# Optimization experiments

Measured on AMD Instinct MI355X. Metric: run time of the kernel, lower is better.

## Reference

```python
import jax, jax.numpy as jnp
import numpy as np

N = 50000      # nodes
E = 800000     # edges per relation
R = 2          # relations
L = 2          # conv layers
D = 128        # hidden / input channels
G = 64         # graphs in batch
C = 8          # num_classes


def setup_inputs() -> dict:
    key = jax.random.key(0)
    ks = jax.random.split(key, 6)
    x = jax.random.normal(ks[0], (N, D), dtype=jnp.float32)
    W = jax.random.normal(ks[1], (L, R, D, D), dtype=jnp.float32) * 0.05
    b = jnp.zeros((L, R, D), dtype=jnp.float32)
    lin_w = jax.random.normal(ks[2], (D, C), dtype=jnp.float32) * 0.05
    lin_b = jnp.zeros((C,), dtype=jnp.float32)
    edge_index = jax.random.randint(ks[3], (R, 2, E), 0, N, dtype=jnp.int32)
    batch = jnp.sort(jax.random.randint(ks[4], (N,), 0, G, dtype=jnp.int32))
    return {"x": x, "W": W, "b": b, "lin_w": lin_w, "lin_b": lin_b,
            "edge_index": edge_index, "batch": batch}


def _gcn_conv(x, src, dst, inv_sqrt_deg, W_r, b_r):
    """PyG GCNConv: symmetric-normalized aggregation with self loops.
    out[i] = sum_{j->i} d_i^-1/2 d_j^-1/2 (x_j W) + d_i^-1 (x_i W) + b
    where d includes the self loop (in-degree + 1)."""
    xw = x @ W_r                                   # [N, D]
    norm = inv_sqrt_deg[src] * inv_sqrt_deg[dst]   # [E]
    agg = jax.ops.segment_sum(xw[src] * norm[:, None], dst, num_segments=N)
    agg = agg + xw * (inv_sqrt_deg * inv_sqrt_deg)[:, None]  # self-loop msg
    return agg + b_r


def reference(x, W, b, lin_w, lin_b, edge_index, batch):
    # Pre-compute per-relation symmetric normalization (same for all layers).
    inv_sqrt_degs = []
    for r in range(R):
        dst = edge_index[r, 1]
        deg = jax.ops.segment_sum(jnp.ones((E,), x.dtype), dst, num_segments=N) + 1.0
        inv_sqrt_degs.append(jax.lax.rsqrt(deg))

    h = x
    for l in range(L):
        out = jnp.zeros((N, D), x.dtype)
        for r in range(R):  # HeteroConv aggr='sum' over relations
            out = out + _gcn_conv(h, edge_index[r, 0], edge_index[r, 1],
                                  inv_sqrt_degs[r], W[l, r], b[l, r])
        h = jax.nn.relu(out) if l < L - 1 else out

    # global_mean_pool over batch ids
    counts = jax.ops.segment_sum(jnp.ones((N,), x.dtype), batch, num_segments=G)
    sums = jax.ops.segment_sum(h, batch, num_segments=G)
    pooled = sums / jnp.maximum(counts, 1.0)[:, None]   # [G, D]
    # dropout(p=0.5) is identity in eval mode; final Linear
    return pooled @ lin_w + lin_b                        # [G, C]
```

## Files before the change

kernel.cpp:

```cpp
#include <hip/hip_runtime.h>
#include <math.h>

#define NN 50000
#define EE 800000
#define RR 2
#define LL 2
#define DD 128
#define GG 64
#define CCLS 8
#define NBUK 196
#define BCAP 6144

typedef unsigned int uint;
typedef unsigned short ushort;
typedef short bf16x8 __attribute__((ext_vector_type(8)));
typedef float f32x4 __attribute__((ext_vector_type(4)));
typedef float f32x2 __attribute__((ext_vector_type(2)));

#define OFF_XW    ((size_t)0)
#define OFF_H1    ((size_t)12800000)
#define OFF_WBT   ((size_t)25600000)
#define OFF_ISD   ((size_t)25731072)
#define OFF_RP    ((size_t)26131072)
#define OFF_CI    ((size_t)26531136)
#define OFF_BD    ((size_t)32931136)
#define OFF_ZERO  ((size_t)42564928)
#define ZO_GCUR 0
#define ZO_SUM  1600
#define ZO_CNT  34368
#define ZERO_BYTES 34624

static __device__ __forceinline__ ushort f2b(float f) {
  uint u = __float_as_uint(f);
  uint r = (u + 0x7fffu + ((u >> 16) & 1u)) >> 16;
  return (ushort)r;
}
static __device__ __forceinline__ float blo(uint u) { return __uint_as_float(u << 16); }
static __device__ __forceinline__ float bhi(uint u) { return __uint_as_float(u & 0xffff0000u); }

__global__ __launch_bounds__(256) void k_wprep(const float* __restrict__ W,
                                               ushort* __restrict__ WT) {
  int idx = blockIdx.x * 256 + threadIdx.x;
  int lr = idx >> 14;
  int rem = idx & 16383;
  int n = rem >> 7, k = rem & 127;
  WT[lr * 16384 + n * 128 + k] = f2b(W[lr * 16384 + k * 128 + n]);
}

__global__ __launch_bounds__(256) void k_part(const int* __restrict__ EI,
                                              int* __restrict__ gcur,
                                              uint* __restrict__ bdata) {
  __shared__ int hist[256];
  __shared__ int sbase[256];
  __shared__ int gbase[256];
  __shared__ int lcur[256];
  __shared__ uint stage[4096];
  __shared__ unsigned char bstage[4096];
  const int r = blockIdx.y;
  const int t = threadIdx.x;
  const int e0 = blockIdx.x * 4096;
  const int cnt = min(4096, EE - e0);
  hist[t] = 0;
  lcur[t] = 0;
  __syncthreads();

  int src[16], dst[16];
  bool val[4];
#pragma unroll
  for (int j = 0; j < 4; ++j) {
    int i4 = (j * 256 + t) * 4;
    val[j] = (i4 < cnt);
    if (val[j]) {
      int4 s4 = *(const int4*)(EI + (size_t)r * 2 * EE + e0 + i4);
      int4 d4 = *(const int4*)(EI + (size_t)r * 2 * EE + EE + e0 + i4);
      src[j * 4 + 0] = s4.x; src[j * 4 + 1] = s4.y; src[j * 4 + 2] = s4.z; src[j * 4 + 3] = s4.w;
      dst[j * 4 + 0] = d4.x; dst[j * 4 + 1] = d4.y; dst[j * 4 + 2] = d4.z; dst[j * 4 + 3] = d4.w;
#pragma unroll
      for (int i = 0; i < 4; ++i) atomicAdd(&hist[dst[j * 4 + i] >> 8], 1);
    }
  }
  __syncthreads();
  int hv = hist[t];
  if (t < NBUK && hv > 0)
    gbase[t] = atomicAdd(&gcur[r * NBUK + t], hv);
  else
    gbase[t] = 0;
  sbase[t] = hv;
  __syncthreads();
  for (int off = 1; off < 256; off <<= 1) {
    int u = (t >= off) ? sbase[t - off] : 0;
    __syncthreads();
    sbase[t] += u;
    __syncthreads();
  }
  int incl = sbase[t];
  hist[t] = incl - hv;
  __syncthreads();
#pragma unroll
  for (int j = 0; j < 4; ++j) {
    if (val[j]) {
#pragma unroll
      for (int i = 0; i < 4; ++i) {
        int d = dst[j * 4 + i];
        int b = d >> 8;
        int p = atomicAdd(&lcur[b], 1);
        int pos = hist[b] + p;
        stage[pos] = ((uint)src[j * 4 + i] << 8) | (uint)(d & 255);
        bstage[pos] = (unsigned char)b;
      }
    }
  }
  __syncthreads();
  for (int s = t; s < cnt; s += 256) {
    int b = (int)bstage[s];
    bdata[(size_t)(r * NBUK + b) * BCAP + gbase[b] + (s - hist[b])] = stage[s];
  }
}

__global__ __launch_bounds__(256) void k_csr(const uint* __restrict__ bdata,
                                             const int* __restrict__ gcur,
                                             float* __restrict__ isd,
                                             int* __restrict__ rp,
                                             int* __restrict__ ci) {
  __shared__ int lcnt[256];
  __shared__ int lrp[256];
  __shared__ int lcur[256];
  __shared__ int cstage[BCAP];
  __shared__ int basesh;
  const int b = blockIdx.x;
  const int r = blockIdx.y;
  const int t = threadIdx.x;
  const int cnt = gcur[r * NBUK + b];
  lcnt[t] = (t < b) ? gcur[r * NBUK + t] : 0;
  __syncthreads();
  for (int off = 128; off > 0; off >>= 1) {
    if (t < off) lcnt[t] += lcnt[t + off];
    __syncthreads();
  }
  if (t == 0) basesh = lcnt[0];
  __syncthreads();
  const int base = basesh;
  const uint* bd = bdata + (size_t)(r * NBUK + b) * BCAP;
  __syncthreads();
  lcnt[t] = 0;
  lcur[t] = 0;
  __syncthreads();
  for (int s = t; s < cnt; s += 256) {
    uint pr = bd[s];
    atomicAdd(&lcnt[pr & 255u], 1);
  }
  __syncthreads();
  int deg = lcnt[t];
  lrp[t] = deg;
  __syncthreads();
  for (int off = 1; off < 256; off <<= 1) {
    int u = (t >= off) ? lrp[t - off] : 0;
    __syncthreads();
    lrp[t] += u;
    __syncthreads();
  }
  int incl = lrp[t];
  __syncthreads();
  lrp[t] = incl - deg;
  __syncthreads();
  int node = b * 256 + t;
  if (node < NN) {
    isd[r * NN + node] = rsqrtf((float)(deg + 1));
    rp[r * (NN + 1) + node] = base + lrp[t];
  }
  if (b == NBUK - 1 && t == 0) rp[r * (NN + 1) + NN] = EE;
  for (int s = t; s < cnt; s += 256) {
    uint pr = bd[s];
    int j = (int)(pr & 255u);
    int p = atomicAdd(&lcur[j], 1);
    cstage[lrp[j] + p] = (int)(pr >> 8);
  }
  __syncthreads();
  for (int s = t; s < cnt; s += 256) ci[(size_t)r * EE + base + s] = cstage[s];
}

#define AL_S 72
#define WT_S 136
template <int IN_BF16>
__global__ __launch_bounds__(256) void k_gemm(const void* __restrict__ Xv,
                                              const ushort* __restrict__ WTg,
                                              const float* __restrict__ isd,
                                              uint* __restrict__ Y) {
  __shared__ ushort WTl[128 * WT_S];
  __shared__ ushort Al[128 * AL_S];
  const int r = blockIdx.y;
  const int m0b = blockIdx.x * 128;
  const int t = threadIdx.x;
  const int w = t >> 6, L = t & 63, q = L >> 4, ln = L & 15;
  uint* Yr = Y + (size_t)r * NN * 32;
  const ushort* WTr = WTg + (size_t)r * 16384;

#pragma unroll
  for (int i = 0; i < 8; ++i) {
    int g = t + i * 256;
    int n = g >> 4, k0 = (g & 15) * 8;
    *(uint4*)(&WTl[n * WT_S + k0]) = *(const uint4*)(WTr + n * 128 + k0);
  }

  f32x4 acc[2][8];
#pragma unroll
  for (int mt = 0; mt < 2; ++mt)
#pragma unroll
    for (int nt = 0; nt < 8; ++nt) {
      acc[mt][nt][0] = 0.f; acc[mt][nt][1] = 0.f;
      acc[mt][nt][2] = 0.f; acc[mt][nt][3] = 0.f;
    }

  for (int hh = 0; hh < 2; ++hh) {
    __syncthreads();
    {
      int row = t >> 1, ch = t & 1;
      int gm = m0b + row;
      ushort* dst = &Al[row * AL_S + ch * 32];
      if (gm < NN) {
        if (IN_BF16) {
          const uint4* xp = (const uint4*)((const ushort*)Xv + (size_t)gm * 128 + hh * 64 + ch * 32);
#pragma unroll
          for (int j = 0; j < 4; ++j) ((uint4*)dst)[j] = xp[j];
        } else {
          const float4* xp = (const float4*)((const float*)Xv + (size_t)gm * 128 + hh * 64 + ch * 32);
          ushort tmp[32];
#pragma unroll
          for (int j = 0; j < 8; ++j) {
            float4 v = xp[j];
            tmp[j * 4 + 0] = f2b(v.x); tmp[j * 4 + 1] = f2b(v.y);
            tmp[j * 4 + 2] = f2b(v.z); tmp[j * 4 + 3] = f2b(v.w);
          }
#pragma unroll
          for (int j = 0; j < 4; ++j) ((uint4*)dst)[j] = ((uint4*)tmp)[j];
        }
      } else {
        uint4 z = make_uint4(0, 0, 0, 0);
#pragma unroll
        for (int j = 0; j < 4; ++j) ((uint4*)dst)[j] = z;
      }
    }
    __syncthreads();
#pragma unroll
    for (int kk = 0; kk < 2; ++kk) {
      bf16x8 b0 = *(const bf16x8*)(&Al[(w * 32 + ln) * AL_S + kk * 32 + q * 8]);
      bf16x8 b1 = *(const bf16x8*)(&Al[(w * 32 + 16 + ln) * AL_S + kk * 32 + q * 8]);
#pragma unroll
      for (int nt = 0; nt < 8; ++nt) {
        bf16x8 a = *(const bf16x8*)(&WTl[(nt * 16 + ln) * WT_S + hh * 64 + kk * 32 + q * 8]);
        acc[0][nt] = __builtin_amdgcn_mfma_f32_16x16x32_bf16(a, b0, acc[0][nt], 0, 0, 0);
        acc[1][nt] = __builtin_amdgcn_mfma_f32_16x16x32_bf16(a, b1, acc[1][nt], 0, 0, 0);
      }
    }
  }
#pragma unroll
  for (int mt = 0; mt < 2; ++mt) {
    int m = m0b + w * 32 + mt * 16 + ln;
    if (m < NN) {
      float sc = isd[r * NN + m];
      uint* yp = Yr + (size_t)m * 32;
#pragma unroll
      for (int nt = 0; nt < 8; ++nt) {
        f32x4 v = acc[mt][nt];
        uint u = __builtin_amdgcn_cvt_pk_fp8_f32(v[0] * sc, v[1] * sc, 0u, false);
        u = __builtin_amdgcn_cvt_pk_fp8_f32(v[2] * sc, v[3] * sc, u, true);
        yp[nt * 4 + q] = u;
      }
    }
  }
}

__global__ __launch_bounds__(256) void k_agg(const uint4* __restrict__ xw4,
                                             const int* __restrict__ rp,
                                             const int* __restrict__ ci,
                                             const float* __restrict__ isd,
                                             const float* __restrict__ bias,
                                             uint* __restrict__ hout, int relu_flag) {
  const int w = threadIdx.x >> 6;
  const int lane = threadIdx.x & 63;
  const int g = lane >> 3, c = lane & 7;
  const int i = blockIdx.x * 4 + w;

  float tot[16];
#pragma unroll
  for (int k = 0; k < 16; ++k) tot[k] = 0.f;

#pragma unroll
  for (int r = 0; r < RR; ++r) {
    const uint4* xwr = xw4 + (size_t)r * NN * 8;
    const int* cir = ci + (size_t)r * EE;
    const float di = isd[r * NN + i];
    const int e0 = rp[r * (NN + 1) + i];
    const int cnt = rp[r * (NN + 1) + i + 1] - e0;
    const int total = cnt + 1;

    float acc[16];
#pragma unroll
    for (int k = 0; k < 16; ++k) acc[k] = 0.f;

    int s_cur = (g < cnt) ? cir[e0 + g] : i;
    for (int base = 0; base < total; base += 8) {
      int idxn = base + 8 + g;
      int s_next = (idxn < cnt) ? cir[e0 + idxn] : i;
      if (base + g < total) {
        uint4 u = xwr[(size_t)s_cur * 8 + c];
        f32x2 v;
        v = __builtin_amdgcn_cvt_pk_f32_fp8(u.x, false); acc[0] += v[0];  acc[1] += v[1];
        v = __builtin_amdgcn_cvt_pk_f32_fp8(u.x, true);  acc[2] += v[0];  acc[3] += v[1];
        v = __builtin_amdgcn_cvt_pk_f32_fp8(u.y, false); acc[4] += v[0];  acc[5] += v[1];
        v = __builtin_amdgcn_cvt_pk_f32_fp8(u.y, true);  acc[6] += v[0];  acc[7] += v[1];
        v = __builtin_amdgcn_cvt_pk_f32_fp8(u.z, false); acc[8] += v[0];  acc[9] += v[1];
        v = __builtin_amdgcn_cvt_pk_f32_fp8(u.z, true);  acc[10] += v[0]; acc[11] += v[1];
        v = __builtin_amdgcn_cvt_pk_f32_fp8(u.w, false); acc[12] += v[0]; acc[13] += v[1];
        v = __builtin_amdgcn_cvt_pk_f32_fp8(u.w, true);  acc[14] += v[0]; acc[15] += v[1];
      }
      s_cur = s_next;
    }
#pragma unroll
    for (int k = 0; k < 16; ++k) tot[k] = fmaf(di, acc[k], tot[k]);
  }

#pragma unroll
  for (int mask = 8; mask <= 32; mask <<= 1) {
#pragma unroll
    for (int k = 0; k < 16; ++k) tot[k] += __shfl_xor(tot[k], mask);
  }

  if (g < 2) {
    int ch0 = c * 16 + g * 8;
    const float4* bp = (const float4*)(bias + ch0);
    const float4* bq = (const float4*)(bias + DD + ch0);
    float4 b0 = bp[0], b1 = bp[1], b2 = bq[0], b3 = bq[1];
    float o[8];
#pragma unroll
    for (int j = 0; j < 8; ++j) o[j] = (g == 0) ? tot[j] : tot[8 + j];
    o[0] += b0.x + b2.x; o[1] += b0.y + b2.y; o[2] += b0.z + b2.z; o[3] += b0.w + b2.w;
    o[4] += b1.x + b3.x; o[5] += b1.y + b3.y; o[6] += b1.z + b3.z; o[7] += b1.w + b3.w;
    if (relu_flag) {
#pragma unroll
      for (int j = 0; j < 8; ++j) o[j] = fmaxf(o[j], 0.f);
    }
    uint4 pk;
    pk.x = (uint)f2b(o[0]) | ((uint)f2b(o[1]) << 16);
    pk.y = (uint)f2b(o[2]) | ((uint)f2b(o[3]) << 16);
    pk.z = (uint)f2b(o[4]) | ((uint)f2b(o[5]) << 16);
    pk.w = (uint)f2b(o[6]) | ((uint)f2b(o[7]) << 16);
    ((uint4*)(hout + (size_t)i * 64))[c * 2 + g] = pk;
  }
}

#define PCHUNK 32
__global__ __launch_bounds__(64) void k_pool(const uint* __restrict__ h,
                                             const int* __restrict__ batch,
                                             float* __restrict__ sums,
                                             int* __restrict__ counts) {
  int lane = threadIdx.x;
  int n0 = blockIdx.x * PCHUNK;
  int n1 = n0 + PCHUNK;
  if (n1 > NN) n1 = NN;
  if (n0 >= NN) return;
  float aLo = 0.f, aHi = 0.f;
  int cnt = 0;
  int g = batch[n0];
  uint u = h[(size_t)n0 * 64 + lane];
  for (int n = n0; n < n1; ++n) {
    uint unext = 0;
    int gnext = g;
    if (n + 1 < n1) {
      unext = h[(size_t)(n + 1) * 64 + lane];
      gnext = batch[n + 1];
    }
    aLo += blo(u);
    aHi += bhi(u);
    cnt++;
    if (n + 1 < n1 && gnext != g) {
      atomicAdd(&sums[g * DD + lane * 2], aLo);
      atomicAdd(&sums[g * DD + lane * 2 + 1], aHi);
      if (lane == 0) atomicAdd(&counts[g], cnt);
      aLo = 0.f; aHi = 0.f; cnt = 0;
      g = gnext;
    }
    u = unext;
  }
  atomicAdd(&sums[g * DD + lane * 2], aLo);
  atomicAdd(&sums[g * DD + lane * 2 + 1], aHi);
  if (lane == 0) atomicAdd(&counts[g], cnt);
}

__global__ __launch_bounds__(512) void k_final(const float* __restrict__ sums,
                                               const int* __restrict__ counts,
                                               const float* __restrict__ lin_w,
                                               const float* __restrict__ lin_b,
                                               float* __restrict__ out) {
  int t = threadIdx.x;
  int g = t >> 3, co = t & 7;
  float cnt = (float)counts[g];
  if (cnt < 1.f) cnt = 1.f;
  float inv = 1.f / cnt;
  float v = lin_b[co];
  for (int d = 0; d < DD; ++d) v += (sums[g * DD + d] * inv) * lin_w[d * CCLS + co];
  out[t] = v;
}

extern "C" void kernel_launch(void* const* d_in, const int* in_sizes, int n_in,
                              void* d_out, int out_size, void* d_ws, size_t ws_size,
                              hipStream_t stream) {
  (void)in_sizes; (void)n_in; (void)out_size; (void)ws_size;
  const float* x     = (const float*)d_in[0];
  const float* W     = (const float*)d_in[1];
  const float* b     = (const float*)d_in[2];
  const float* lin_w = (const float*)d_in[3];
  const float* lin_b = (const float*)d_in[4];
  const int*   EI    = (const int*)d_in[5];
  const int*   batch = (const int*)d_in[6];
  float* out = (float*)d_out;

  char* ws = (char*)d_ws;
  uint*   xw    = (uint*)(ws + OFF_XW);
  uint*   h1    = (uint*)(ws + OFF_H1);
  ushort* WbfT  = (ushort*)(ws + OFF_WBT);
  float*  isd   = (float*)(ws + OFF_ISD);
  int*    rp    = (int*)(ws + OFF_RP);
  int*    ci    = (int*)(ws + OFF_CI);
  uint*   bdata = (uint*)(ws + OFF_BD);
  char*   zb    = ws + OFF_ZERO;
  int*    gcur  = (int*)(zb + ZO_GCUR);
  float*  sums  = (float*)(zb + ZO_SUM);
  int*    counts= (int*)(zb + ZO_CNT);

  (void)hipMemsetAsync(zb, 0, ZERO_BYTES, stream);

  k_wprep<<<256, 256, 0, stream>>>(W, WbfT);
  k_part<<<dim3((EE + 4095) / 4096, RR), 256, 0, stream>>>(EI, gcur, bdata);
  k_csr<<<dim3(NBUK, RR), 256, 0, stream>>>(bdata, gcur, isd, rp, ci);

  for (int l = 0; l < LL; ++l) {
    const ushort* WTl_g = WbfT + (size_t)l * RR * DD * DD;
    if (l == 0)
      k_gemm<0><<<dim3((NN + 127) / 128, RR), 256, 0, stream>>>((const void*)x, WTl_g, isd, xw);
    else
      k_gemm<1><<<dim3((NN + 127) / 128, RR), 256, 0, stream>>>((const void*)h1, WTl_g, isd, xw);
    k_agg<<<(NN + 3) / 4, 256, 0, stream>>>((const uint4*)xw, rp, ci, isd,
                                            b + (size_t)l * RR * DD, h1,
                                            (l < LL - 1) ? 1 : 0);
  }
  k_pool<<<(NN + PCHUNK - 1) / PCHUNK, 64, 0, stream>>>(h1, batch, sums, counts);
  k_final<<<1, GG * CCLS, 0, stream>>>(sums, counts, lin_w, lin_b, out);
}
```

Measured before the change: 258.5 us.

## Pad CSR rows to multiples of four with a zero dummy node and branchless gather

The CSR build now pads each node's neighbour list, including the self loop, to a multiple of four, using a dummy node NN whose transformed row is written as zero by the GEMM. Each bucket gets a fixed-stride region, so the global prefix over buckets is removed. The aggregation kernel uses 16 lanes per edge with 8-byte fp8 loads over 4 edges per step, without bounds checks, and pipelines the next index and row load. The cost is extra padded gathers and larger index storage; the xw buffer also now shares its workspace with the bucket staging area.

Result: slower. 289.3 us (+11.9%).

```diff
diff --git a/kernel.cpp b/kernel.cpp
--- a/kernel.cpp
+++ b/kernel.cpp
@@ -10,6 +10,7 @@
 #define CCLS 8
 #define NBUK 196
 #define BCAP 6144
+#define BCI  7424
 
 typedef unsigned int uint;
 typedef unsigned short ushort;
@@ -17,14 +18,14 @@
 typedef float f32x4 __attribute__((ext_vector_type(4)));
 typedef float f32x2 __attribute__((ext_vector_type(2)));
 
-#define OFF_XW    ((size_t)0)
-#define OFF_H1    ((size_t)12800000)
-#define OFF_WBT   ((size_t)25600000)
-#define OFF_ISD   ((size_t)25731072)
-#define OFF_RP    ((size_t)26131072)
-#define OFF_CI    ((size_t)26531136)
-#define OFF_BD    ((size_t)32931136)
-#define OFF_ZERO  ((size_t)42564928)
+#define OFF_H1    ((size_t)0)
+#define OFF_WBT   ((size_t)12800000)
+#define OFF_ISD   ((size_t)12931072)
+#define OFF_RP    ((size_t)13331072)
+#define OFF_CI    ((size_t)14131072)
+#define OFF_ZERO  ((size_t)25771904)
+#define OFF_BD    ((size_t)25806592)
+#define OFF_XW    ((size_t)25806592)
 #define ZO_GCUR 0
 #define ZO_SUM  1600
 #define ZO_CNT  34368
@@ -120,38 +121,29 @@
 __global__ __launch_bounds__(256) void k_csr(const uint* __restrict__ bdata,
                                              const int* __restrict__ gcur,
                                              float* __restrict__ isd,
-                                             int* __restrict__ rp,
+                                             int* __restrict__ rps,
+                                             int* __restrict__ rpc,
                                              int* __restrict__ ci) {
   __shared__ int lcnt[256];
   __shared__ int lrp[256];
   __shared__ int lcur[256];
-  __shared__ int cstage[BCAP];
-  __shared__ int basesh;
+  __shared__ int cstage[BCI];
+  __shared__ int shtot;
   const int b = blockIdx.x;
   const int r = blockIdx.y;
   const int t = threadIdx.x;
   const int cnt = gcur[r * NBUK + b];
-  lcnt[t] = (t < b) ? gcur[r * NBUK + t] : 0;
-  __syncthreads();
-  for (int off = 128; off > 0; off >>= 1) {
-    if (t < off) lcnt[t] += lcnt[t + off];
-    __syncthreads();
-  }
-  if (t == 0) basesh = lcnt[0];
-  __syncthreads();
-  const int base = basesh;
   const uint* bd = bdata + (size_t)(r * NBUK + b) * BCAP;
-  __syncthreads();
   lcnt[t] = 0;
   lcur[t] = 0;
   __syncthreads();
-  for (int s = t; s < cnt; s += 256) {
-    uint pr = bd[s];
-    atomicAdd(&lcnt[pr & 255u], 1);
-  }
-  __syncthreads();
-  int deg = lcnt[t];
-  lrp[t] = deg;
+  for (int s = t; s < cnt; s += 256) atomicAdd(&lcnt[bd[s] & 255u], 1);
+  __syncthreads();
+  const int deg = lcnt[t];
+  const int node = b * 256 + t;
+  const int valid = (node < NN) ? 1 : 0;
+  const int deg3 = valid ? ((deg + 1 + 3) & ~3) : 0;
+  lrp[t] = deg3;
   __syncthreads();
   for (int off = 1; off < 256; off <<= 1) {
     int u = (t >= off) ? lrp[t - off] : 0;
@@ -160,15 +152,21 @@
     __syncthreads();
   }
   int incl = lrp[t];
-  __syncthreads();
-  lrp[t] = incl - deg;
-  __syncthreads();
-  int node = b * 256 + t;
-  if (node < NN) {
+  if (t == 255) shtot = incl;
+  __syncthreads();
+  lrp[t] = incl - deg3;
+  __syncthreads();
+  const int ex = lrp[t];
+  if (valid) {
     isd[r * NN + node] = rsqrtf((float)(deg + 1));
-    rp[r * (NN + 1) + node] = base + lrp[t];
-  }
-  if (b == NBUK - 1 && t == 0) rp[r * (NN + 1) + NN] = EE;
+    rps[r * NN + node] = b * BCI + ex;
+    rpc[r * NN + node] = deg3;
+    cstage[ex + deg] = node;
+    for (int p = deg + 1; p < deg3; ++p) cstage[ex + p] = NN;
+  }
+  const int btot = shtot;
+  if (t < 16) cstage[btot + t] = NN;
+  __syncthreads();
   for (int s = t; s < cnt; s += 256) {
     uint pr = bd[s];
     int j = (int)(pr & 255u);
@@ -176,7 +174,9 @@
     cstage[lrp[j] + p] = (int)(pr >> 8);
   }
   __syncthreads();
-  for (int s = t; s < cnt; s += 256) ci[(size_t)r * EE + base + s] = cstage[s];
+  const int on = btot + 16;
+  int* co = ci + (size_t)r * (NBUK * BCI) + (size_t)b * BCI;
+  for (int s = t; s < on; s += 256) co[s] = cstage[s];
 }
 
 #define AL_S 72
@@ -192,7 +192,7 @@
   const int m0b = blockIdx.x * 128;
   const int t = threadIdx.x;
   const int w = t >> 6, L = t & 63, q = L >> 4, ln = L & 15;
-  uint* Yr = Y + (size_t)r * NN * 32;
+  uint* Yr = Y + (size_t)r * (NN + 1) * 32;
   const ushort* WTr = WTg + (size_t)r * 16384;
 
 #pragma unroll
@@ -256,8 +256,8 @@
 #pragma unroll
   for (int mt = 0; mt < 2; ++mt) {
     int m = m0b + w * 32 + mt * 16 + ln;
-    if (m < NN) {
-      float sc = isd[r * NN + m];
+    if (m <= NN) {
+      float sc = (m < NN) ? isd[r * NN + m] : 0.f;
       uint* yp = Yr + (size_t)m * 32;
 #pragma unroll
       for (int nt = 0; nt < 8; ++nt) {
@@ -270,72 +270,76 @@
   }
 }
 
-__global__ __launch_bounds__(256) void k_agg(const uint4* __restrict__ xw4,
-                                             const int* __restrict__ rp,
+__global__ __launch_bounds__(256) void k_agg(const char* __restrict__ xw,
+                                             const int* __restrict__ rps,
+                                             const int* __restrict__ rpc,
                                              const int* __restrict__ ci,
                                              const float* __restrict__ isd,
                                              const float* __restrict__ bias,
                                              uint* __restrict__ hout, int relu_flag) {
   const int w = threadIdx.x >> 6;
   const int lane = threadIdx.x & 63;
-  const int g = lane >> 3, c = lane & 7;
+  const int g = lane >> 4, c = lane & 15;
   const int i = blockIdx.x * 4 + w;
-
-  float tot[16];
-#pragma unroll
-  for (int k = 0; k < 16; ++k) tot[k] = 0.f;
+  const uint cb = (uint)c * 8u;
+
+  f32x2 tot[4];
+#pragma unroll
+  for (int j = 0; j < 4; ++j) { tot[j][0] = 0.f; tot[j][1] = 0.f; }
 
 #pragma unroll
   for (int r = 0; r < RR; ++r) {
-    const uint4* xwr = xw4 + (size_t)r * NN * 8;
-    const int* cir = ci + (size_t)r * EE;
+    const char* xwr = xw + (size_t)r * ((size_t)(NN + 1) * 128);
+    const int e0 = rps[r * NN + i];
+    const int total = rpc[r * NN + i];
+    const int* ce = ci + (size_t)r * (NBUK * BCI) + e0;
     const float di = isd[r * NN + i];
-    const int e0 = rp[r * (NN + 1) + i];
-    const int cnt = rp[r * (NN + 1) + i + 1] - e0;
-    const int total = cnt + 1;
-
-    float acc[16];
-#pragma unroll
-    for (int k = 0; k < 16; ++k) acc[k] = 0.f;
-
-    int s_cur = (g < cnt) ? cir[e0 + g] : i;
-    for (int base = 0; base < total; base += 8) {
-      int idxn = base + 8 + g;
-      int s_next = (idxn < cnt) ? cir[e0 + idxn] : i;
-      if (base + g < total) {
-        uint4 u = xwr[(size_t)s_cur * 8 + c];
-        f32x2 v;
-        v = __builtin_amdgcn_cvt_pk_f32_fp8(u.x, false); acc[0] += v[0];  acc[1] += v[1];
-        v = __builtin_amdgcn_cvt_pk_f32_fp8(u.x, true);  acc[2] += v[0];  acc[3] += v[1];
-        v = __builtin_amdgcn_cvt_pk_f32_fp8(u.y, false); acc[4] += v[0];  acc[5] += v[1];
-        v = __builtin_amdgcn_cvt_pk_f32_fp8(u.y, true);  acc[6] += v[0];  acc[7] += v[1];
-        v = __builtin_amdgcn_cvt_pk_f32_fp8(u.z, false); acc[8] += v[0];  acc[9] += v[1];
-        v = __builtin_amdgcn_cvt_pk_f32_fp8(u.z, true);  acc[10] += v[0]; acc[11] += v[1];
-        v = __builtin_amdgcn_cvt_pk_f32_fp8(u.w, false); acc[12] += v[0]; acc[13] += v[1];
-        v = __builtin_amdgcn_cvt_pk_f32_fp8(u.w, true);  acc[14] += v[0]; acc[15] += v[1];
-      }
-      s_cur = s_next;
-    }
-#pragma unroll
-    for (int k = 0; k < 16; ++k) tot[k] = fmaf(di, acc[k], tot[k]);
-  }
-
-#pragma unroll
-  for (int mask = 8; mask <= 32; mask <<= 1) {
-#pragma unroll
-    for (int k = 0; k < 16; ++k) tot[k] += __shfl_xor(tot[k], mask);
-  }
-
-  if (g < 2) {
-    int ch0 = c * 16 + g * 8;
-    const float4* bp = (const float4*)(bias + ch0);
-    const float4* bq = (const float4*)(bias + DD + ch0);
-    float4 b0 = bp[0], b1 = bp[1], b2 = bq[0], b3 = bq[1];
-    float o[8];
-#pragma unroll
-    for (int j = 0; j < 8; ++j) o[j] = (g == 0) ? tot[j] : tot[8 + j];
-    o[0] += b0.x + b2.x; o[1] += b0.y + b2.y; o[2] += b0.z + b2.z; o[3] += b0.w + b2.w;
-    o[4] += b1.x + b3.x; o[5] += b1.y + b3.y; o[6] += b1.z + b3.z; o[7] += b1.w + b3.w;
+
+    f32x2 acc[4];
+#pragma unroll
+    for (int j = 0; j < 4; ++j) { acc[j][0] = 0.f; acc[j][1] = 0.f; }
+
+    int s0 = ce[g];
+    uint2 ucur = *(const uint2*)(xwr + (((uint)s0 << 7) + cb));
+    int s1 = ce[4 + g];
+    int ip = 8 + g;
+    for (int base = 0; base < total; base += 4) {
+      uint2 unext = *(const uint2*)(xwr + (((uint)s1 << 7) + cb));
+      int s2 = ce[ip];
+      ip += 4;
+      f32x2 v;
+      v = __builtin_amdgcn_cvt_pk_f32_fp8(ucur.x, false); acc[0] += v;
+      v = __builtin_amdgcn_cvt_pk_f32_fp8(ucur.x, true);  acc[1] += v;
+      v = __builtin_amdgcn_cvt_pk_f32_fp8(ucur.y, false); acc[2] += v;
+      v = __builtin_amdgcn_cvt_pk_f32_fp8(ucur.y, true);  acc[3] += v;
+      ucur = unext;
+      s1 = s2;
+    }
+    f32x2 d2; d2[0] = di; d2[1] = di;
+#pragma unroll
+    for (int j = 0; j < 4; ++j) tot[j] += acc[j] * d2;
+  }
+
+#pragma unroll
+  for (int mask = 16; mask <= 32; mask <<= 1) {
+#pragma unroll
+    for (int j = 0; j < 4; ++j) {
+      f32x2 o;
+      o[0] = __shfl_xor(tot[j][0], mask);
+      o[1] = __shfl_xor(tot[j][1], mask);
+      tot[j] += o;
+    }
+  }
+
+  if (g == 0) {
+    const int ch0 = c * 8;
+    const float4* b0p = (const float4*)(bias + ch0);
+    const float4* b1p = (const float4*)(bias + DD + ch0);
+    float4 ba = b0p[0], bb = b0p[1], bc = b1p[0], bd = b1p[1];
+    float o[8] = {tot[0][0], tot[0][1], tot[1][0], tot[1][1],
+                  tot[2][0], tot[2][1], tot[3][0], tot[3][1]};
+    o[0] += ba.x + bc.x; o[1] += ba.y + bc.y; o[2] += ba.z + bc.z; o[3] += ba.w + bc.w;
+    o[4] += bb.x + bd.x; o[5] += bb.y + bd.y; o[6] += bb.z + bd.z; o[7] += bb.w + bd.w;
     if (relu_flag) {
 #pragma unroll
       for (int j = 0; j < 8; ++j) o[j] = fmaxf(o[j], 0.f);
@@ -345,7 +349,7 @@
     pk.y = (uint)f2b(o[2]) | ((uint)f2b(o[3]) << 16);
     pk.z = (uint)f2b(o[4]) | ((uint)f2b(o[5]) << 16);
     pk.w = (uint)f2b(o[6]) | ((uint)f2b(o[7]) << 16);
-    ((uint4*)(hout + (size_t)i * 64))[c * 2 + g] = pk;
+    ((uint4*)(hout + (size_t)i * 64))[c] = pk;
   }
 }
 
@@ -416,13 +420,14 @@
   float* out = (float*)d_out;
 
   char* ws = (char*)d_ws;
-  uint*   xw    = (uint*)(ws + OFF_XW);
   uint*   h1    = (uint*)(ws + OFF_H1);
   ushort* WbfT  = (ushort*)(ws + OFF_WBT);
   float*  isd   = (float*)(ws + OFF_ISD);
-  int*    rp    = (int*)(ws + OFF_RP);
+  int*    rps   = (int*)(ws + OFF_RP);
+  int*    rpc   = rps + 2 * NN;
   int*    ci    = (int*)(ws + OFF_CI);
   uint*   bdata = (uint*)(ws + OFF_BD);
+  uint*   xw    = (uint*)(ws + OFF_XW);
   char*   zb    = ws + OFF_ZERO;
   int*    gcur  = (int*)(zb + ZO_GCUR);
   float*  sums  = (float*)(zb + ZO_SUM);
@@ -432,7 +437,7 @@
 
   k_wprep<<<256, 256, 0, stream>>>(W, WbfT);
   k_part<<<dim3((EE + 4095) / 4096, RR), 256, 0, stream>>>(EI, gcur, bdata);
-  k_csr<<<dim3(NBUK, RR), 256, 0, stream>>>(bdata, gcur, isd, rp, ci);
+  k_csr<<<dim3(NBUK, RR), 256, 0, stream>>>(bdata, gcur, isd, rps, rpc, ci);
 
   for (int l = 0; l < LL; ++l) {
     const ushort* WTl_g = WbfT + (size_t)l * RR * DD * DD;
@@ -440,7 +445,7 @@
       k_gemm<0><<<dim3((NN + 127) / 128, RR), 256, 0, stream>>>((const void*)x, WTl_g, isd, xw);
     else
       k_gemm<1><<<dim3((NN + 127) / 128, RR), 256, 0, stream>>>((const void*)h1, WTl_g, isd, xw);
-    k_agg<<<(NN + 3) / 4, 256, 0, stream>>>((const uint4*)xw, rp, ci, isd,
+    k_agg<<<(NN + 3) / 4, 256, 0, stream>>>((const char*)xw, rps, rpc, ci, isd,
                                             b + (size_t)l * RR * DD, h1,
                                             (l < LL - 1) ? 1 : 0);
   }
```

## Share input tile across relations in GEMM and parallelize final linear

Applied to the files above, without the earlier changes.

The GEMM now loads the full 128x128 input tile into shared memory once per block and loops over both relations, streaming each relation's weight half-tiles, instead of launching a separate block per relation that reloads the input. This halves input reads and the fp32-to-bf16 conversion work in layer 0, at the cost of half as many blocks and more weight reloads per block. The final linear layer is also split across 64 blocks, with a shuffle reduction replacing the serial 128-step loop in one block.

Measured after the change: 254.8 us (median of 2 runs). About the same (-1.4%).

```diff
diff --git a/kernel.cpp b/kernel.cpp
--- a/kernel.cpp
+++ b/kernel.cpp
@@ -179,92 +179,93 @@
   for (int s = t; s < cnt; s += 256) ci[(size_t)r * EE + base + s] = cstage[s];
 }
 
-#define AL_S 72
-#define WT_S 136
+#define AL2_S 136
+#define WT2_S 72
 template <int IN_BF16>
 __global__ __launch_bounds__(256) void k_gemm(const void* __restrict__ Xv,
                                               const ushort* __restrict__ WTg,
                                               const float* __restrict__ isd,
                                               uint* __restrict__ Y) {
-  __shared__ ushort WTl[128 * WT_S];
-  __shared__ ushort Al[128 * AL_S];
-  const int r = blockIdx.y;
+  __shared__ ushort Al[128 * AL2_S];
+  __shared__ ushort WTl[128 * WT2_S];
   const int m0b = blockIdx.x * 128;
   const int t = threadIdx.x;
   const int w = t >> 6, L = t & 63, q = L >> 4, ln = L & 15;
-  uint* Yr = Y + (size_t)r * NN * 32;
-  const ushort* WTr = WTg + (size_t)r * 16384;
-
-#pragma unroll
-  for (int i = 0; i < 8; ++i) {
-    int g = t + i * 256;
-    int n = g >> 4, k0 = (g & 15) * 8;
-    *(uint4*)(&WTl[n * WT_S + k0]) = *(const uint4*)(WTr + n * 128 + k0);
-  }
-
-  f32x4 acc[2][8];
-#pragma unroll
-  for (int mt = 0; mt < 2; ++mt)
-#pragma unroll
-    for (int nt = 0; nt < 8; ++nt) {
-      acc[mt][nt][0] = 0.f; acc[mt][nt][1] = 0.f;
-      acc[mt][nt][2] = 0.f; acc[mt][nt][3] = 0.f;
-    }
-
-  for (int hh = 0; hh < 2; ++hh) {
-    __syncthreads();
-    {
-      int row = t >> 1, ch = t & 1;
-      int gm = m0b + row;
-      ushort* dst = &Al[row * AL_S + ch * 32];
-      if (gm < NN) {
-        if (IN_BF16) {
-          const uint4* xp = (const uint4*)((const ushort*)Xv + (size_t)gm * 128 + hh * 64 + ch * 32);
-#pragma unroll
-          for (int j = 0; j < 4; ++j) ((uint4*)dst)[j] = xp[j];
-        } else {
-          const float4* xp = (const float4*)((const float*)Xv + (size_t)gm * 128 + hh * 64 + ch * 32);
-          ushort tmp[32];
-#pragma unroll
-          for (int j = 0; j < 8; ++j) {
-            float4 v = xp[j];
-            tmp[j * 4 + 0] = f2b(v.x); tmp[j * 4 + 1] = f2b(v.y);
-            tmp[j * 4 + 2] = f2b(v.z); tmp[j * 4 + 3] = f2b(v.w);
-          }
-#pragma unroll
-          for (int j = 0; j < 4; ++j) ((uint4*)dst)[j] = ((uint4*)tmp)[j];
+
+  {
+    int row = t >> 1, ch0 = (t & 1) * 64;
+    int gm = m0b + row;
+    ushort* dst = &Al[row * AL2_S + ch0];
+    if (gm < NN) {
+      if (IN_BF16) {
+        const uint4* xp = (const uint4*)((const ushort*)Xv + (size_t)gm * 128 + ch0);
+#pragma unroll
+        for (int j = 0; j < 8; ++j) ((uint4*)dst)[j] = xp[j];
+      } else {
+        const float4* xp = (const float4*)((const float*)Xv + (size_t)gm * 128 + ch0);
+#pragma unroll
+        for (int j = 0; j < 16; ++j) {
+          float4 v = xp[j];
+          dst[j * 4 + 0] = f2b(v.x); dst[j * 4 + 1] = f2b(v.y);
+          dst[j * 4 + 2] = f2b(v.z); dst[j * 4 + 3] = f2b(v.w);
         }
-      } else {
-        uint4 z = make_uint4(0, 0, 0, 0);
-#pragma unroll
-        for (int j = 0; j < 4; ++j) ((uint4*)dst)[j] = z;
-      }
-    }
-    __syncthreads();
-#pragma unroll
-    for (int kk = 0; kk < 2; ++kk) {
-      bf16x8 b0 = *(const bf16x8*)(&Al[(w * 32 + ln) * AL_S + kk * 32 + q * 8]);
-      bf16x8 b1 = *(const bf16x8*)(&Al[(w * 32 + 16 + ln) * AL_S + kk * 32 + q * 8]);
+      }
+    } else {
+      uint4 z = make_uint4(0, 0, 0, 0);
+#pragma unroll
+      for (int j = 0; j < 8; ++j) ((uint4*)dst)[j] = z;
+    }
+  }
+
+#pragma unroll
+  for (int r = 0; r < RR; ++r) {
+    const ushort* WTr = WTg + (size_t)r * 16384;
+    uint* Yr = Y + (size_t)r * NN * 32;
+
+    f32x4 acc[2][8];
+#pragma unroll
+    for (int mt = 0; mt < 2; ++mt)
 #pragma unroll
       for (int nt = 0; nt < 8; ++nt) {
-        bf16x8 a = *(const bf16x8*)(&WTl[(nt * 16 + ln) * WT_S + hh * 64 + kk * 32 + q * 8]);
-        acc[0][nt] = __builtin_amdgcn_mfma_f32_16x16x32_bf16(a, b0, acc[0][nt], 0, 0, 0);
-        acc[1][nt] = __builtin_amdgcn_mfma_f32_16x16x32_bf16(a, b1, acc[1][nt], 0, 0, 0);
-      }
-    }
-  }
-#pragma unroll
-  for (int mt = 0; mt < 2; ++mt) {
-    int m = m0b + w * 32 + mt * 16 + ln;
-    if (m < NN) {
-      float sc = isd[r * NN + m];
-      uint* yp = Yr + (size_t)m * 32;
-#pragma unroll
-      for (int nt = 0; nt < 8; ++nt) {
-        f32x4 v = acc[mt][nt];
-        uint u = __builtin_amdgcn_cvt_pk_fp8_f32(v[0] * sc, v[1] * sc, 0u, false);
-        u = __builtin_amdgcn_cvt_pk_fp8_f32(v[2] * sc, v[3] * sc, u, true);
-        yp[nt * 4 + q] = u;
+        acc[mt][nt][0] = 0.f; acc[mt][nt][1] = 0.f;
+        acc[mt][nt][2] = 0.f; acc[mt][nt][3] = 0.f;
+      }
+
+    for (int hh = 0; hh < 2; ++hh) {
+      __syncthreads();
+      {
+        int n = t >> 1, k0 = (t & 1) * 32;
+#pragma unroll
+        for (int j = 0; j < 4; ++j)
+          *(uint4*)(&WTl[n * WT2_S + k0 + j * 8]) =
+              *(const uint4*)(WTr + n * 128 + hh * 64 + k0 + j * 8);
+      }
+      __syncthreads();
+#pragma unroll
+      for (int kk = 0; kk < 2; ++kk) {
+        bf16x8 b0 = *(const bf16x8*)(&Al[(w * 32 + ln) * AL2_S + hh * 64 + kk * 32 + q * 8]);
+        bf16x8 b1 = *(const bf16x8*)(&Al[(w * 32 + 16 + ln) * AL2_S + hh * 64 + kk * 32 + q * 8]);
+#pragma unroll
+        for (int nt = 0; nt < 8; ++nt) {
+          bf16x8 a = *(const bf16x8*)(&WTl[(nt * 16 + ln) * WT2_S + kk * 32 + q * 8]);
+          acc[0][nt] = __builtin_amdgcn_mfma_f32_16x16x32_bf16(a, b0, acc[0][nt], 0, 0, 0);
+          acc[1][nt] = __builtin_amdgcn_mfma_f32_16x16x32_bf16(a, b1, acc[1][nt], 0, 0, 0);
+        }
+      }
+    }
+#pragma unroll
+    for (int mt = 0; mt < 2; ++mt) {
+      int m = m0b + w * 32 + mt * 16 + ln;
+      if (m < NN) {
+        float sc = isd[r * NN + m];
+        uint* yp = Yr + (size_t)m * 32;
+#pragma unroll
+        for (int nt = 0; nt < 8; ++nt) {
+          f32x4 v = acc[mt][nt];
+          uint u = __builtin_amdgcn_cvt_pk_fp8_f32(v[0] * sc, v[1] * sc, 0u, false);
+          u = __builtin_amdgcn_cvt_pk_fp8_f32(v[2] * sc, v[3] * sc, u, true);
+          yp[nt * 4 + q] = u;
+        }
       }
     }
   }
@@ -387,19 +388,27 @@
   if (lane == 0) atomicAdd(&counts[g], cnt);
 }
 
-__global__ __launch_bounds__(512) void k_final(const float* __restrict__ sums,
-                                               const int* __restrict__ counts,
-                                               const float* __restrict__ lin_w,
-                                               const float* __restrict__ lin_b,
-                                               float* __restrict__ out) {
-  int t = threadIdx.x;
-  int g = t >> 3, co = t & 7;
-  float cnt = (float)counts[g];
-  if (cnt < 1.f) cnt = 1.f;
-  float inv = 1.f / cnt;
-  float v = lin_b[co];
-  for (int d = 0; d < DD; ++d) v += (sums[g * DD + d] * inv) * lin_w[d * CCLS + co];
-  out[t] = v;
+__global__ __launch_bounds__(64) void k_final(const float* __restrict__ sums,
+                                              const int* __restrict__ counts,
+                                              const float* __restrict__ lin_w,
+                                              const float* __restrict__ lin_b,
+                                              float* __restrict__ out) {
+  const int g = blockIdx.x;
+  const int t = threadIdx.x;
+  const int co = t & 7, dp = t >> 3;
+  float p = 0.f;
+#pragma unroll
+  for (int j = 0; j < 16; ++j) {
+    int d = dp + 8 * j;
+    p += sums[g * DD + d] * lin_w[d * CCLS + co];
+  }
+#pragma unroll
+  for (int mask = 8; mask <= 32; mask <<= 1) p += __shfl_xor(p, mask);
+  if (t < 8) {
+    float cnt = (float)counts[g];
+    if (cnt < 1.f) cnt = 1.f;
+    out[g * CCLS + t] = p / cnt + lin_b[t];
+  }
 }
 
 extern "C" void kernel_launch(void* const* d_in, const int* in_sizes, int n_in,
@@ -437,13 +446,13 @@
   for (int l = 0; l < LL; ++l) {
     const ushort* WTl_g = WbfT + (size_t)l * RR * DD * DD;
     if (l == 0)
-      k_gemm<0><<<dim3((NN + 127) / 128, RR), 256, 0, stream>>>((const void*)x, WTl_g, isd, xw);
+      k_gemm<0><<<(NN + 127) / 128, 256, 0, stream>>>((const void*)x, WTl_g, isd, xw);
     else
-      k_gemm<1><<<dim3((NN + 127) / 128, RR), 256, 0, stream>>>((const void*)h1, WTl_g, isd, xw);
+      k_gemm<1><<<(NN + 127) / 128, 256, 0, stream>>>((const void*)h1, WTl_g, isd, xw);
     k_agg<<<(NN + 3) / 4, 256, 0, stream>>>((const uint4*)xw, rp, ci, isd,
                                             b + (size_t)l * RR * DD, h1,
                                             (l < LL - 1) ? 1 : 0);
   }
   k_pool<<<(NN + PCHUNK - 1) / PCHUNK, 64, 0, stream>>>(h1, batch, sums, counts);
-  k_final<<<1, GG * CCLS, 0, stream>>>(sums, counts, lin_w, lin_b, out);
-}
+  k_final<<<GG, 64, 0, stream>>>(sums, counts, lin_w, lin_b, out);
+}
```
